# Kernel optimization log

Hardware: AMD Instinct MI355X
Metric: run time of the kernel (lower is better)

Reference implementation:

```python
import jax, jax.numpy as jnp
import numpy as np

WH, WW = 7, 7
N = WH * WW
NH = 6
HEAD_DIM = 192 // NH
W_RES = 56
R_MAX = 4 * 56  # patch_size[0] * H
PI = 3.141592653589793


def _rel_coords():
    ch, cw = np.arange(WH), np.arange(WW)
    coords = np.stack(np.meshgrid(ch, cw, indexing='ij'))  # (2, WH, WW)
    flat = coords.reshape(2, -1)
    rel = flat[:, :, None] - flat[:, None, :]  # (2, N, N)
    radius = rel[0]   # in [-(WH-1), WH-1]
    azimuth = rel[1]  # in [-(WW-1), WW-1]
    return radius, azimuth


def setup_inputs() -> dict:
    key = jax.random.key(0)
    ks = jax.random.split(key, 10)
    B_ = 2048
    dim = 192
    return {
        'x': jax.random.normal(ks[0], (B_, N, dim), jnp.float32),
        'D': jax.random.uniform(ks[1], (B_, 1), jnp.float32),
        'qkv_w': jax.random.normal(ks[2], (3 * dim, dim), jnp.float32) * 0.02,
        'qkv_b': jax.random.normal(ks[3], (3 * dim,), jnp.float32) * 0.02,
        'proj_w': jax.random.normal(ks[4], (dim, dim), jnp.float32) * 0.02,
        'proj_b': jax.random.normal(ks[5], (dim,), jnp.float32) * 0.02,
        'a_p': jax.random.normal(ks[6], (2 * WW - 1, NH), jnp.float32) * 0.02,
        'b_p': jax.random.normal(ks[7], (2 * WW - 1, NH), jnp.float32) * 0.02,
        'a_r': jax.random.normal(ks[8], (2 * WH - 1, NH), jnp.float32) * 0.02,
        'b_r': jax.random.normal(ks[9], (2 * WH - 1, NH), jnp.float32) * 0.02,
    }


def reference(x, D, qkv_w, qkv_b, proj_w, proj_b, a_p, b_p, a_r, b_r):
    B_, n, C = x.shape
    radius_np, azimuth_np = _rel_coords()
    # torch a_r[radius] with negative ints wraps like python indexing; emulate via modulo
    rad_idx = jnp.asarray(radius_np % (2 * WH - 1))
    az_idx = jnp.asarray(azimuth_np % (2 * WW - 1))
    radius = jnp.asarray(radius_np, jnp.float32)   # (N, N)
    azimuth = jnp.asarray(azimuth_np, jnp.float32)  # (N, N)

    scale = HEAD_DIM ** -0.5
    qkv = (x @ qkv_w.T + qkv_b).reshape(B_, n, 3, NH, HEAD_DIM)
    qkv = jnp.transpose(qkv, (2, 0, 3, 1, 4))  # (3, B_, NH, N, hd)
    q, k, v = qkv[0] * scale, qkv[1], qkv[2]

    attn = jnp.einsum('bhnd,bhmd->bhnm', q, k)  # (B_, NH, N, N)

    # azimuthal bias: (N, N, NH) -> (NH, N, N)
    az = azimuth * (2.0 * PI / W_RES)
    A_phi = a_p[az_idx] * jnp.cos(az)[..., None] + b_p[az_idx] * jnp.sin(az)[..., None]
    A_phi = jnp.transpose(A_phi, (2, 0, 1))  # (NH, N, N)

    # radial bias: D (B_,1) scales radius -> (B_, N, N); combine -> (B_, NH, N, N)
    rad = D[:, 0][:, None, None] * radius[None]  # (B_, N, N)
    ang = rad * (2.0 * PI / R_MAX)
    A_r = (a_r[rad_idx][None] * jnp.cos(ang)[..., None]
           + b_r[rad_idx][None] * jnp.sin(ang)[..., None])  # (B_, N, N, NH)
    A_r = jnp.transpose(A_r, (0, 3, 1, 2))  # (B_, NH, N, N)

    attn = jax.nn.softmax(attn + A_phi[None] + A_r, axis=-1)
    out = jnp.einsum('bhnm,bhmd->bhnd', attn, v)
    out = jnp.transpose(out, (0, 2, 1, 3)).reshape(B_, n, C)
    return out @ proj_w.T + proj_b
```

## Files before the change

kernel.cpp:

```cpp
#include <hip/hip_runtime.h>

#define NTOK 49
#define NH 6
#define HD 32
#define DIM 192
#define QKV_DIM 576
#define PI_F 3.14159265358979323846f
#define XSTR 204

typedef __bf16 bf16_t;
typedef __bf16 bf16x4 __attribute__((ext_vector_type(4)));
typedef __bf16 bf16x8 __attribute__((ext_vector_type(8)));
typedef float f32x4 __attribute__((ext_vector_type(4)));

__global__ __launch_bounds__(256) void cvt_weights(const float* __restrict__ qkv_w,
                                                   const float* __restrict__ proj_w,
                                                   bf16_t* __restrict__ wq,
                                                   bf16_t* __restrict__ wp) {
    int idx = blockIdx.x * 256 + threadIdx.x;
    if (idx < QKV_DIM * DIM) {
        wq[idx] = (bf16_t)qkv_w[idx];
    } else {
        int j = idx - QKV_DIM * DIM;
        if (j < DIM * DIM) wp[j] = (bf16_t)proj_w[j];
    }
}

__device__ __forceinline__ int2 pack4(float a, float b, float c, float d) {
    bf16x4 t = { (bf16_t)a, (bf16_t)b, (bf16_t)c, (bf16_t)d };
    union { bf16x4 v; int2 i; } u;
    u.v = t;
    return u.i;
}

__device__ __forceinline__ bf16x8 asm_frag(int2 p0, int2 p1, int src_lo, bool sel_hi) {
    int a0x = __shfl(p0.x, src_lo),      a0y = __shfl(p0.y, src_lo);
    int a1x = __shfl(p0.x, src_lo + 16), a1y = __shfl(p0.y, src_lo + 16);
    int b0x = __shfl(p1.x, src_lo),      b0y = __shfl(p1.y, src_lo);
    int b1x = __shfl(p1.x, src_lo + 16), b1y = __shfl(p1.y, src_lo + 16);
    union { int x[4]; bf16x8 v; } u;
    u.x[0] = sel_hi ? b0x : a0x;
    u.x[1] = sel_hi ? b0y : a0y;
    u.x[2] = sel_hi ? b1x : a1x;
    u.x[3] = sel_hi ? b1y : a1y;
    return u.v;
}

__global__ __launch_bounds__(768, 3) void fused_win_attn(
        const float* __restrict__ x,
        const float* __restrict__ Dp,
        const bf16_t* __restrict__ wq,
        const float* __restrict__ qkv_b,
        const bf16_t* __restrict__ wp,
        const float* __restrict__ proj_b,
        const float* __restrict__ a_p,
        const float* __restrict__ b_p,
        const float* __restrict__ a_r,
        const float* __restrict__ b_r,
        float* __restrict__ out,
        int nwin) {
    __shared__ __align__(16) bf16_t sh_xo[2][49 * XSTR];
    __shared__ float bias_sh[12][169];

    const int tid  = threadIdx.x;
    const int w    = tid >> 6;
    const int lane = tid & 63;
    const int l16  = lane & 15;
    const int quad = lane >> 4;
    const int wb   = w / 6;
    const int h    = w % 6;
    const int win  = blockIdx.x * 2 + wb;
    const int winc = min(win, nwin - 1);
    const bool alive = (win < nwin);

    bf16_t* xl     = sh_xo[wb];
    float*  bias13 = bias_sh[w];

    for (int u = tid; u < 4704; u += 768) {
        int wbs = (u >= 2352) ? 1 : 0;
        int e = (u - wbs * 2352) * 4;
        int r = e / 192, c = e % 192;
        int wsrc = min(blockIdx.x * 2 + wbs, nwin - 1);
        float4 xv = *(const float4*)(x + (size_t)wsrc * (NTOK * DIM) + e);
        bf16x4 pk = { (bf16_t)xv.x, (bf16_t)xv.y, (bf16_t)xv.z, (bf16_t)xv.w };
        *(bf16x4*)(&sh_xo[wbs][r * XSTR + c]) = pk;
    }

    const float Dv = Dp[winc];
    for (int u = lane; u < 169; u += 64) {
        int dr = u / 13 - 6, da = u % 13 - 6;
        int ri = (dr < 0) ? dr + 13 : dr;
        int ai = (da < 0) ? da + 13 : da;
        float ang_a = (float)da * (2.0f * PI_F / 56.0f);
        float ang_r = Dv * (float)dr * (2.0f * PI_F / 448.0f);
        bias13[u] = a_p[ai * NH + h] * __cosf(ang_a) + b_p[ai * NH + h] * __sinf(ang_a)
                  + a_r[ri * NH + h] * __cosf(ang_r) + b_r[ri * NH + h] * __sinf(ang_r);
    }
    __syncthreads();

    int xoff[4];
#pragma unroll
    for (int mt = 0; mt < 4; ++mt) {
        int row = mt * 16 + l16;
        xoff[mt] = min(row, 48) * XSTR + quad * 8;
    }

    const int src_lo  = ((lane >> 4) & 1) * 32 + l16;
    const bool sel_hi = (lane & 32) != 0;

    const float scale = 0.17677669529663687f;
    int2 qp[4][2], kp[4][2];
    {
        const bf16_t* wgq = wq + (size_t)(h * 32) * DIM;
        const bf16_t* wgk = wq + (size_t)(DIM + h * 32) * DIM;
        f32x4 qa[4][2] = {}, ka[4][2] = {};
#pragma unroll
        for (int ks = 0; ks < 6; ++ks) {
            bf16x8 wq0 = *(const bf16x8*)(wgq + (size_t)l16 * DIM + ks * 32 + quad * 8);
            bf16x8 wq1 = *(const bf16x8*)(wgq + (size_t)(16 + l16) * DIM + ks * 32 + quad * 8);
            bf16x8 wk0 = *(const bf16x8*)(wgk + (size_t)l16 * DIM + ks * 32 + quad * 8);
            bf16x8 wk1 = *(const bf16x8*)(wgk + (size_t)(16 + l16) * DIM + ks * 32 + quad * 8);
#pragma unroll
            for (int mt = 0; mt < 4; ++mt) {
                bf16x8 xf = *(const bf16x8*)(&xl[xoff[mt] + ks * 32]);
                qa[mt][0] = __builtin_amdgcn_mfma_f32_16x16x32_bf16(wq0, xf, qa[mt][0], 0, 0, 0);
                qa[mt][1] = __builtin_amdgcn_mfma_f32_16x16x32_bf16(wq1, xf, qa[mt][1], 0, 0, 0);
                ka[mt][0] = __builtin_amdgcn_mfma_f32_16x16x32_bf16(wk0, xf, ka[mt][0], 0, 0, 0);
                ka[mt][1] = __builtin_amdgcn_mfma_f32_16x16x32_bf16(wk1, xf, ka[mt][1], 0, 0, 0);
            }
        }
        float4 bq0 = *(const float4*)(qkv_b + h * 32 + quad * 4);
        float4 bq1 = *(const float4*)(qkv_b + h * 32 + 16 + quad * 4);
        float4 bk0 = *(const float4*)(qkv_b + DIM + h * 32 + quad * 4);
        float4 bk1 = *(const float4*)(qkv_b + DIM + h * 32 + 16 + quad * 4);
#pragma unroll
        for (int mt = 0; mt < 4; ++mt) {
            qp[mt][0] = pack4((qa[mt][0][0] + bq0.x) * scale, (qa[mt][0][1] + bq0.y) * scale,
                              (qa[mt][0][2] + bq0.z) * scale, (qa[mt][0][3] + bq0.w) * scale);
            qp[mt][1] = pack4((qa[mt][1][0] + bq1.x) * scale, (qa[mt][1][1] + bq1.y) * scale,
                              (qa[mt][1][2] + bq1.z) * scale, (qa[mt][1][3] + bq1.w) * scale);
            kp[mt][0] = pack4(ka[mt][0][0] + bk0.x, ka[mt][0][1] + bk0.y,
                              ka[mt][0][2] + bk0.z, ka[mt][0][3] + bk0.w);
            kp[mt][1] = pack4(ka[mt][1][0] + bk1.x, ka[mt][1][1] + bk1.y,
                              ka[mt][1][2] + bk1.z, ka[mt][1][3] + bk1.w);
        }
    }

    int2 vp[4][2];
    {
        const bf16_t* wgv = wq + (size_t)(2 * DIM + h * 32) * DIM;
        f32x4 va[4][2] = {};
#pragma unroll
        for (int ks = 0; ks < 6; ++ks) {
            bf16x8 wv0 = *(const bf16x8*)(wgv + (size_t)l16 * DIM + ks * 32 + quad * 8);
            bf16x8 wv1 = *(const bf16x8*)(wgv + (size_t)(16 + l16) * DIM + ks * 32 + quad * 8);
#pragma unroll
            for (int mt = 0; mt < 4; ++mt) {
                bf16x8 xf = *(const bf16x8*)(&xl[xoff[mt] + ks * 32]);
                va[mt][0] = __builtin_amdgcn_mfma_f32_16x16x32_bf16(xf, wv0, va[mt][0], 0, 0, 0);
                va[mt][1] = __builtin_amdgcn_mfma_f32_16x16x32_bf16(xf, wv1, va[mt][1], 0, 0, 0);
            }
        }
        float bv0 = qkv_b[2 * DIM + h * 32 + l16];
        float bv1 = qkv_b[2 * DIM + h * 32 + 16 + l16];
#pragma unroll
        for (int mt = 0; mt < 4; ++mt) {
            vp[mt][0] = pack4(va[mt][0][0] + bv0, va[mt][0][1] + bv0,
                              va[mt][0][2] + bv0, va[mt][0][3] + bv0);
            vp[mt][1] = pack4(va[mt][1][0] + bv1, va[mt][1][1] + bv1,
                              va[mt][1][2] + bv1, va[mt][1][3] + bv1);
        }
    }

    bf16x8 qf[4], kf[4];
#pragma unroll
    for (int t = 0; t < 4; ++t) {
        qf[t] = asm_frag(qp[t][0], qp[t][1], src_lo, sel_hi);
        kf[t] = asm_frag(kp[t][0], kp[t][1], src_lo, sel_hi);
    }
    bf16x8 vf[2][2];
#pragma unroll
    for (int kt = 0; kt < 2; ++kt)
#pragma unroll
        for (int ntd = 0; ntd < 2; ++ntd)
            vf[ntd][kt] = asm_frag(vp[2 * kt][ntd], vp[2 * kt + 1][ntd], src_lo, sel_hi);

    int jcp[4];
#pragma unroll
    for (int nt = 0; nt < 4; ++nt) {
        int p = 0;
#pragma unroll
        for (int r = 0; r < 4; ++r) {
            int j = nt * 16 + quad * 4 + r;
            p |= ((j / 7) * 13 + (j % 7)) << (8 * r);
        }
        jcp[nt] = p;
    }

    __syncthreads();

    for (int mt = 0; mt < 4; ++mt) {
        f32x4 s[4] = {};
#pragma unroll
        for (int nt = 0; nt < 4; ++nt)
            s[nt] = __builtin_amdgcn_mfma_f32_16x16x32_bf16(kf[nt], qf[mt], s[nt], 0, 0, 0);

        int i = mt * 16 + l16;
        int icl = min(i, 48);
        int icode = (icl / 7) * 13 + (icl % 7) + 84;

        float val[4][4];
        float mx = -1e30f;
#pragma unroll
        for (int nt = 0; nt < 4; ++nt)
#pragma unroll
            for (int r = 0; r < 4; ++r) {
                int j = nt * 16 + quad * 4 + r;
                int idx = icode - ((jcp[nt] >> (8 * r)) & 255);
                idx = max(idx, 0);
                float vv = s[nt][r] + bias13[idx];
                vv = (j < 49) ? vv : -1e30f;
                val[nt][r] = vv;
                mx = fmaxf(mx, vv);
            }
        mx = fmaxf(mx, __shfl_xor(mx, 16));
        mx = fmaxf(mx, __shfl_xor(mx, 32));
        float sum = 0.f;
#pragma unroll
        for (int nt = 0; nt < 4; ++nt)
#pragma unroll
            for (int r = 0; r < 4; ++r) {
                float e = __expf(val[nt][r] - mx);
                val[nt][r] = e;
                sum += e;
            }
        sum += __shfl_xor(sum, 16);
        sum += __shfl_xor(sum, 32);
        float rs = 1.0f / sum;

        int2 pv0 = pack4(val[0][0], val[0][1], val[0][2], val[0][3]);
        int2 pv1 = pack4(val[1][0], val[1][1], val[1][2], val[1][3]);
        int2 pv2 = pack4(val[2][0], val[2][1], val[2][2], val[2][3]);
        int2 pv3 = pack4(val[3][0], val[3][1], val[3][2], val[3][3]);
        bf16x8 pT0 = asm_frag(pv0, pv1, src_lo, sel_hi);
        bf16x8 pT1 = asm_frag(pv2, pv3, src_lo, sel_hi);

        f32x4 o0 = {}, o1 = {};
        o0 = __builtin_amdgcn_mfma_f32_16x16x32_bf16(vf[0][0], pT0, o0, 0, 0, 0);
        o0 = __builtin_amdgcn_mfma_f32_16x16x32_bf16(vf[0][1], pT1, o0, 0, 0, 0);
        o1 = __builtin_amdgcn_mfma_f32_16x16x32_bf16(vf[1][0], pT0, o1, 0, 0, 0);
        o1 = __builtin_amdgcn_mfma_f32_16x16x32_bf16(vf[1][1], pT1, o1, 0, 0, 0);

        if (i < 49) {
            *(int2*)(&xl[i * XSTR + h * 32 + quad * 4]) =
                pack4(o0[0] * rs, o0[1] * rs, o0[2] * rs, o0[3] * rs);
            *(int2*)(&xl[i * XSTR + h * 32 + 16 + quad * 4]) =
                pack4(o1[0] * rs, o1[1] * rs, o1[2] * rs, o1[3] * rs);
        }
    }

    __syncthreads();

    bf16x8 wf[2][6];
#pragma unroll
    for (int nt = 0; nt < 2; ++nt)
#pragma unroll
        for (int ks = 0; ks < 6; ++ks)
            wf[nt][ks] = *(const bf16x8*)(wp + (size_t)(h * 32 + nt * 16 + l16) * DIM + ks * 32 + quad * 8);

    f32x4 pacc[4][2] = {};
#pragma unroll
    for (int mt = 0; mt < 4; ++mt)
#pragma unroll
        for (int ks = 0; ks < 6; ++ks) {
            bf16x8 oa = *(const bf16x8*)(&xl[xoff[mt] + ks * 32]);
            pacc[mt][0] = __builtin_amdgcn_mfma_f32_16x16x32_bf16(oa, wf[0][ks], pacc[mt][0], 0, 0, 0);
            pacc[mt][1] = __builtin_amdgcn_mfma_f32_16x16x32_bf16(oa, wf[1][ks], pacc[mt][1], 0, 0, 0);
        }

    float pb0 = proj_b[h * 32 + l16];
    float pb1 = proj_b[h * 32 + 16 + l16];
#pragma unroll
    for (int mt = 0; mt < 4; ++mt)
#pragma unroll
        for (int r = 0; r < 4; ++r) {
            int i = mt * 16 + quad * 4 + r;
            if (alive && i < 49) {
                float* op = out + ((size_t)win * NTOK + i) * DIM + h * 32;
                op[l16]      = pacc[mt][0][r] + pb0;
                op[16 + l16] = pacc[mt][1][r] + pb1;
            }
        }
}

extern "C" void kernel_launch(void* const* d_in, const int* in_sizes, int n_in,
                              void* d_out, int out_size, void* d_ws, size_t ws_size,
                              hipStream_t stream) {
    const float* x      = (const float*)d_in[0];
    const float* D      = (const float*)d_in[1];
    const float* qkv_w  = (const float*)d_in[2];
    const float* qkv_b  = (const float*)d_in[3];
    const float* proj_w = (const float*)d_in[4];
    const float* proj_b = (const float*)d_in[5];
    const float* a_p    = (const float*)d_in[6];
    const float* b_p    = (const float*)d_in[7];
    const float* a_r    = (const float*)d_in[8];
    const float* b_r    = (const float*)d_in[9];
    float* out = (float*)d_out;

    const int B_ = in_sizes[0] / (NTOK * DIM);

    char* wsp = (char*)d_ws;
    bf16_t* wq = (bf16_t*)wsp; wsp += (size_t)QKV_DIM * DIM * 2;
    bf16_t* wp = (bf16_t*)wsp;

    cvt_weights<<<dim3((QKV_DIM * DIM + DIM * DIM + 255) / 256), dim3(256), 0, stream>>>(
        qkv_w, proj_w, wq, wp);

    fused_win_attn<<<dim3((B_ + 1) / 2), dim3(768), 0, stream>>>(
        x, D, wq, qkv_b, wp, proj_b, a_p, b_p, a_r, b_r, out, B_);
}
```

Baseline: 295.6 us.

## Use 16x16x16 MFMA to drop lane shuffles, swizzle LDS, fuse QKV loops

Replaces the shuffle-based fragment reassembly (asm_frag) by switching the attention-score and PV matmuls to 16x16x16 bf16 MFMAs, whose operand layout matches the accumulator output of the projection, so no cross-lane shuffles are needed. The padded shared-memory stride is replaced by an XOR swizzle on an unpadded layout to avoid bank conflicts. The Q/K/V projection loops are merged so each x fragment is read once from LDS, and the proj weight loads are hoisted before the barrier. Risks are higher register pressure from holding Q, K and V accumulators at the same time, and twice as many MFMA instructions, each smaller, in the attention part.

```diff
diff --git a/kernel.cpp b/kernel.cpp
--- a/kernel.cpp
+++ b/kernel.cpp
@@ -2,16 +2,15 @@
 
 #define NTOK 49
 #define NH 6
-#define HD 32
 #define DIM 192
 #define QKV_DIM 576
 #define PI_F 3.14159265358979323846f
-#define XSTR 204
 
 typedef __bf16 bf16_t;
 typedef __bf16 bf16x4 __attribute__((ext_vector_type(4)));
 typedef __bf16 bf16x8 __attribute__((ext_vector_type(8)));
 typedef float f32x4 __attribute__((ext_vector_type(4)));
+typedef short s16x4 __attribute__((ext_vector_type(4)));
 
 __global__ __launch_bounds__(256) void cvt_weights(const float* __restrict__ qkv_w,
                                                    const float* __restrict__ proj_w,
@@ -26,24 +25,15 @@
     }
 }
 
-__device__ __forceinline__ int2 pack4(float a, float b, float c, float d) {
+__device__ __forceinline__ int swz(int r, int c) {
+    return r * DIM + (((c >> 3) ^ (r & 7)) << 3) + (c & 7);
+}
+
+__device__ __forceinline__ s16x4 pack4s(float a, float b, float c, float d) {
     bf16x4 t = { (bf16_t)a, (bf16_t)b, (bf16_t)c, (bf16_t)d };
-    union { bf16x4 v; int2 i; } u;
+    union { bf16x4 v; s16x4 s; } u;
     u.v = t;
-    return u.i;
-}
-
-__device__ __forceinline__ bf16x8 asm_frag(int2 p0, int2 p1, int src_lo, bool sel_hi) {
-    int a0x = __shfl(p0.x, src_lo),      a0y = __shfl(p0.y, src_lo);
-    int a1x = __shfl(p0.x, src_lo + 16), a1y = __shfl(p0.y, src_lo + 16);
-    int b0x = __shfl(p1.x, src_lo),      b0y = __shfl(p1.y, src_lo);
-    int b1x = __shfl(p1.x, src_lo + 16), b1y = __shfl(p1.y, src_lo + 16);
-    union { int x[4]; bf16x8 v; } u;
-    u.x[0] = sel_hi ? b0x : a0x;
-    u.x[1] = sel_hi ? b0y : a0y;
-    u.x[2] = sel_hi ? b1x : a1x;
-    u.x[3] = sel_hi ? b1y : a1y;
-    return u.v;
+    return u.s;
 }
 
 __global__ __launch_bounds__(768, 3) void fused_win_attn(
@@ -59,7 +49,7 @@
         const float* __restrict__ b_r,
         float* __restrict__ out,
         int nwin) {
-    __shared__ __align__(16) bf16_t sh_xo[2][49 * XSTR];
+    __shared__ __align__(16) bf16_t sh_xo[2][NTOK * DIM];
     __shared__ float bias_sh[12][169];
 
     const int tid  = threadIdx.x;
@@ -83,7 +73,7 @@
         int wsrc = min(blockIdx.x * 2 + wbs, nwin - 1);
         float4 xv = *(const float4*)(x + (size_t)wsrc * (NTOK * DIM) + e);
         bf16x4 pk = { (bf16_t)xv.x, (bf16_t)xv.y, (bf16_t)xv.z, (bf16_t)xv.w };
-        *(bf16x4*)(&sh_xo[wbs][r * XSTR + c]) = pk;
+        *(bf16x4*)(&sh_xo[wbs][swz(r, c)]) = pk;
     }
 
     const float Dv = Dp[winc];
@@ -98,92 +88,59 @@
     }
     __syncthreads();
 
-    int xoff[4];
-#pragma unroll
-    for (int mt = 0; mt < 4; ++mt) {
-        int row = mt * 16 + l16;
-        xoff[mt] = min(row, 48) * XSTR + quad * 8;
-    }
-
-    const int src_lo  = ((lane >> 4) & 1) * 32 + l16;
-    const bool sel_hi = (lane & 32) != 0;
+    int rowc[4];
+#pragma unroll
+    for (int mt = 0; mt < 4; ++mt)
+        rowc[mt] = min(mt * 16 + l16, 48);
 
     const float scale = 0.17677669529663687f;
-    int2 qp[4][2], kp[4][2];
+    s16x4 qp[4][2], kp[4][2], vp[4][2];
     {
         const bf16_t* wgq = wq + (size_t)(h * 32) * DIM;
         const bf16_t* wgk = wq + (size_t)(DIM + h * 32) * DIM;
-        f32x4 qa[4][2] = {}, ka[4][2] = {};
+        const bf16_t* wgv = wq + (size_t)(2 * DIM + h * 32) * DIM;
+        f32x4 qa[4][2] = {}, ka[4][2] = {}, va[4][2] = {};
 #pragma unroll
         for (int ks = 0; ks < 6; ++ks) {
             bf16x8 wq0 = *(const bf16x8*)(wgq + (size_t)l16 * DIM + ks * 32 + quad * 8);
             bf16x8 wq1 = *(const bf16x8*)(wgq + (size_t)(16 + l16) * DIM + ks * 32 + quad * 8);
             bf16x8 wk0 = *(const bf16x8*)(wgk + (size_t)l16 * DIM + ks * 32 + quad * 8);
             bf16x8 wk1 = *(const bf16x8*)(wgk + (size_t)(16 + l16) * DIM + ks * 32 + quad * 8);
+            bf16x8 wv0 = *(const bf16x8*)(wgv + (size_t)l16 * DIM + ks * 32 + quad * 8);
+            bf16x8 wv1 = *(const bf16x8*)(wgv + (size_t)(16 + l16) * DIM + ks * 32 + quad * 8);
 #pragma unroll
             for (int mt = 0; mt < 4; ++mt) {
-                bf16x8 xf = *(const bf16x8*)(&xl[xoff[mt] + ks * 32]);
+                bf16x8 xf = *(const bf16x8*)(&xl[swz(rowc[mt], ks * 32 + quad * 8)]);
                 qa[mt][0] = __builtin_amdgcn_mfma_f32_16x16x32_bf16(wq0, xf, qa[mt][0], 0, 0, 0);
                 qa[mt][1] = __builtin_amdgcn_mfma_f32_16x16x32_bf16(wq1, xf, qa[mt][1], 0, 0, 0);
                 ka[mt][0] = __builtin_amdgcn_mfma_f32_16x16x32_bf16(wk0, xf, ka[mt][0], 0, 0, 0);
                 ka[mt][1] = __builtin_amdgcn_mfma_f32_16x16x32_bf16(wk1, xf, ka[mt][1], 0, 0, 0);
+                va[mt][0] = __builtin_amdgcn_mfma_f32_16x16x32_bf16(xf, wv0, va[mt][0], 0, 0, 0);
+                va[mt][1] = __builtin_amdgcn_mfma_f32_16x16x32_bf16(xf, wv1, va[mt][1], 0, 0, 0);
             }
         }
         float4 bq0 = *(const float4*)(qkv_b + h * 32 + quad * 4);
         float4 bq1 = *(const float4*)(qkv_b + h * 32 + 16 + quad * 4);
         float4 bk0 = *(const float4*)(qkv_b + DIM + h * 32 + quad * 4);
         float4 bk1 = *(const float4*)(qkv_b + DIM + h * 32 + 16 + quad * 4);
-#pragma unroll
-        for (int mt = 0; mt < 4; ++mt) {
-            qp[mt][0] = pack4((qa[mt][0][0] + bq0.x) * scale, (qa[mt][0][1] + bq0.y) * scale,
-                              (qa[mt][0][2] + bq0.z) * scale, (qa[mt][0][3] + bq0.w) * scale);
-            qp[mt][1] = pack4((qa[mt][1][0] + bq1.x) * scale, (qa[mt][1][1] + bq1.y) * scale,
-                              (qa[mt][1][2] + bq1.z) * scale, (qa[mt][1][3] + bq1.w) * scale);
-            kp[mt][0] = pack4(ka[mt][0][0] + bk0.x, ka[mt][0][1] + bk0.y,
-                              ka[mt][0][2] + bk0.z, ka[mt][0][3] + bk0.w);
-            kp[mt][1] = pack4(ka[mt][1][0] + bk1.x, ka[mt][1][1] + bk1.y,
-                              ka[mt][1][2] + bk1.z, ka[mt][1][3] + bk1.w);
-        }
-    }
-
-    int2 vp[4][2];
-    {
-        const bf16_t* wgv = wq + (size_t)(2 * DIM + h * 32) * DIM;
-        f32x4 va[4][2] = {};
-#pragma unroll
-        for (int ks = 0; ks < 6; ++ks) {
-            bf16x8 wv0 = *(const bf16x8*)(wgv + (size_t)l16 * DIM + ks * 32 + quad * 8);
-            bf16x8 wv1 = *(const bf16x8*)(wgv + (size_t)(16 + l16) * DIM + ks * 32 + quad * 8);
-#pragma unroll
-            for (int mt = 0; mt < 4; ++mt) {
-                bf16x8 xf = *(const bf16x8*)(&xl[xoff[mt] + ks * 32]);
-                va[mt][0] = __builtin_amdgcn_mfma_f32_16x16x32_bf16(xf, wv0, va[mt][0], 0, 0, 0);
-                va[mt][1] = __builtin_amdgcn_mfma_f32_16x16x32_bf16(xf, wv1, va[mt][1], 0, 0, 0);
-            }
-        }
         float bv0 = qkv_b[2 * DIM + h * 32 + l16];
         float bv1 = qkv_b[2 * DIM + h * 32 + 16 + l16];
 #pragma unroll
         for (int mt = 0; mt < 4; ++mt) {
-            vp[mt][0] = pack4(va[mt][0][0] + bv0, va[mt][0][1] + bv0,
-                              va[mt][0][2] + bv0, va[mt][0][3] + bv0);
-            vp[mt][1] = pack4(va[mt][1][0] + bv1, va[mt][1][1] + bv1,
-                              va[mt][1][2] + bv1, va[mt][1][3] + bv1);
-        }
-    }
-
-    bf16x8 qf[4], kf[4];
-#pragma unroll
-    for (int t = 0; t < 4; ++t) {
-        qf[t] = asm_frag(qp[t][0], qp[t][1], src_lo, sel_hi);
-        kf[t] = asm_frag(kp[t][0], kp[t][1], src_lo, sel_hi);
-    }
-    bf16x8 vf[2][2];
-#pragma unroll
-    for (int kt = 0; kt < 2; ++kt)
-#pragma unroll
-        for (int ntd = 0; ntd < 2; ++ntd)
-            vf[ntd][kt] = asm_frag(vp[2 * kt][ntd], vp[2 * kt + 1][ntd], src_lo, sel_hi);
+            qp[mt][0] = pack4s((qa[mt][0][0] + bq0.x) * scale, (qa[mt][0][1] + bq0.y) * scale,
+                               (qa[mt][0][2] + bq0.z) * scale, (qa[mt][0][3] + bq0.w) * scale);
+            qp[mt][1] = pack4s((qa[mt][1][0] + bq1.x) * scale, (qa[mt][1][1] + bq1.y) * scale,
+                               (qa[mt][1][2] + bq1.z) * scale, (qa[mt][1][3] + bq1.w) * scale);
+            kp[mt][0] = pack4s(ka[mt][0][0] + bk0.x, ka[mt][0][1] + bk0.y,
+                               ka[mt][0][2] + bk0.z, ka[mt][0][3] + bk0.w);
+            kp[mt][1] = pack4s(ka[mt][1][0] + bk1.x, ka[mt][1][1] + bk1.y,
+                               ka[mt][1][2] + bk1.z, ka[mt][1][3] + bk1.w);
+            vp[mt][0] = pack4s(va[mt][0][0] + bv0, va[mt][0][1] + bv0,
+                               va[mt][0][2] + bv0, va[mt][0][3] + bv0);
+            vp[mt][1] = pack4s(va[mt][1][0] + bv1, va[mt][1][1] + bv1,
+                               va[mt][1][2] + bv1, va[mt][1][3] + bv1);
+        }
+    }
 
     int jcp[4];
 #pragma unroll
@@ -197,13 +154,22 @@
         jcp[nt] = p;
     }
 
+    bf16x8 wf[2][6];
+#pragma unroll
+    for (int nt = 0; nt < 2; ++nt)
+#pragma unroll
+        for (int ks = 0; ks < 6; ++ks)
+            wf[nt][ks] = *(const bf16x8*)(wp + (size_t)(h * 32 + nt * 16 + l16) * DIM + ks * 32 + quad * 8);
+
     __syncthreads();
 
     for (int mt = 0; mt < 4; ++mt) {
         f32x4 s[4] = {};
 #pragma unroll
-        for (int nt = 0; nt < 4; ++nt)
-            s[nt] = __builtin_amdgcn_mfma_f32_16x16x32_bf16(kf[nt], qf[mt], s[nt], 0, 0, 0);
+        for (int nt = 0; nt < 4; ++nt) {
+            s[nt] = __builtin_amdgcn_mfma_f32_16x16x16bf16_1k(kp[nt][0], qp[mt][0], s[nt], 0, 0, 0);
+            s[nt] = __builtin_amdgcn_mfma_f32_16x16x16bf16_1k(kp[nt][1], qp[mt][1], s[nt], 0, 0, 0);
+        }
 
         int i = mt * 16 + l16;
         int icl = min(i, 48);
@@ -238,42 +204,34 @@
         sum += __shfl_xor(sum, 32);
         float rs = 1.0f / sum;
 
-        int2 pv0 = pack4(val[0][0], val[0][1], val[0][2], val[0][3]);
-        int2 pv1 = pack4(val[1][0], val[1][1], val[1][2], val[1][3]);
-        int2 pv2 = pack4(val[2][0], val[2][1], val[2][2], val[2][3]);
-        int2 pv3 = pack4(val[3][0], val[3][1], val[3][2], val[3][3]);
-        bf16x8 pT0 = asm_frag(pv0, pv1, src_lo, sel_hi);
-        bf16x8 pT1 = asm_frag(pv2, pv3, src_lo, sel_hi);
+        s16x4 pvs[4];
+#pragma unroll
+        for (int nt = 0; nt < 4; ++nt)
+            pvs[nt] = pack4s(val[nt][0], val[nt][1], val[nt][2], val[nt][3]);
 
         f32x4 o0 = {}, o1 = {};
-        o0 = __builtin_amdgcn_mfma_f32_16x16x32_bf16(vf[0][0], pT0, o0, 0, 0, 0);
-        o0 = __builtin_amdgcn_mfma_f32_16x16x32_bf16(vf[0][1], pT1, o0, 0, 0, 0);
-        o1 = __builtin_amdgcn_mfma_f32_16x16x32_bf16(vf[1][0], pT0, o1, 0, 0, 0);
-        o1 = __builtin_amdgcn_mfma_f32_16x16x32_bf16(vf[1][1], pT1, o1, 0, 0, 0);
+#pragma unroll
+        for (int kt = 0; kt < 4; ++kt) {
+            o0 = __builtin_amdgcn_mfma_f32_16x16x16bf16_1k(vp[kt][0], pvs[kt], o0, 0, 0, 0);
+            o1 = __builtin_amdgcn_mfma_f32_16x16x16bf16_1k(vp[kt][1], pvs[kt], o1, 0, 0, 0);
+        }
 
         if (i < 49) {
-            *(int2*)(&xl[i * XSTR + h * 32 + quad * 4]) =
-                pack4(o0[0] * rs, o0[1] * rs, o0[2] * rs, o0[3] * rs);
-            *(int2*)(&xl[i * XSTR + h * 32 + 16 + quad * 4]) =
-                pack4(o1[0] * rs, o1[1] * rs, o1[2] * rs, o1[3] * rs);
+            *(s16x4*)(&xl[swz(i, h * 32 + quad * 4)]) =
+                pack4s(o0[0] * rs, o0[1] * rs, o0[2] * rs, o0[3] * rs);
+            *(s16x4*)(&xl[swz(i, h * 32 + 16 + quad * 4)]) =
+                pack4s(o1[0] * rs, o1[1] * rs, o1[2] * rs, o1[3] * rs);
         }
     }
 
     __syncthreads();
 
-    bf16x8 wf[2][6];
-#pragma unroll
-    for (int nt = 0; nt < 2; ++nt)
-#pragma unroll
-        for (int ks = 0; ks < 6; ++ks)
-            wf[nt][ks] = *(const bf16x8*)(wp + (size_t)(h * 32 + nt * 16 + l16) * DIM + ks * 32 + quad * 8);
-
     f32x4 pacc[4][2] = {};
 #pragma unroll
     for (int mt = 0; mt < 4; ++mt)
 #pragma unroll
         for (int ks = 0; ks < 6; ++ks) {
-            bf16x8 oa = *(const bf16x8*)(&xl[xoff[mt] + ks * 32]);
+            bf16x8 oa = *(const bf16x8*)(&xl[swz(rowc[mt], ks * 32 + quad * 8)]);
             pacc[mt][0] = __builtin_amdgcn_mfma_f32_16x16x32_bf16(oa, wf[0][ks], pacc[mt][0], 0, 0, 0);
             pacc[mt][1] = __builtin_amdgcn_mfma_f32_16x16x32_bf16(oa, wf[1][ks], pacc[mt][1], 0, 0, 0);
         }
```

Measured after the change: 254.7 us. 1.16x faster.
